# Optimization experiments

Measured on AMD Instinct MI355X. Metric: run time of the kernel, lower is better.

Reference implementation:

```python
import jax, jax.numpy as jnp
import numpy as np

SAMPLE_THRESH = 0.05  # self.sample_thresh


def grid_sample_bilinear_zeros(img, pts):
    """torch.nn.functional.grid_sample with mode='bilinear', align_corners=False,
    padding_mode='zeros'. img: [C, H, W]; pts: [N, 2] with (x, y) in [-1, 1].
    Returns [C, N]."""
    C, H, W = img.shape
    # align_corners=False unnormalization
    x = (pts[:, 0] + 1.0) * (W / 2.0) - 0.5
    y = (pts[:, 1] + 1.0) * (H / 2.0) - 0.5
    x0 = jnp.floor(x)
    y0 = jnp.floor(y)
    wx1 = x - x0
    wy1 = y - y0
    wx0 = 1.0 - wx1
    wy0 = 1.0 - wy1

    def gather(xi, yi):
        valid = (xi >= 0) & (xi < W) & (yi >= 0) & (yi < H)
        xi_c = jnp.clip(xi, 0, W - 1).astype(jnp.int32)
        yi_c = jnp.clip(yi, 0, H - 1).astype(jnp.int32)
        v = img[:, yi_c, xi_c]  # [C, N]
        return v * valid.astype(img.dtype)[None, :]

    out = (gather(x0, y0) * (wx0 * wy0)[None, :]
           + gather(x0 + 1, y0) * (wx1 * wy0)[None, :]
           + gather(x0, y0 + 1) * (wx0 * wy1)[None, :]
           + gather(x0 + 1, y0 + 1) * (wx1 * wy1)[None, :])
    return out


def setup_inputs() -> dict:
    key = jax.random.key(0)
    k1, k2, k3, k4 = jax.random.split(key, 4)
    N_A, N_B = 8192, 8192
    H, W2 = 504, 1008  # warp is [hs, 2*ws, 4] per post_process
    x_A = jax.random.uniform(k1, (N_A, 2), jnp.float32, -1.0, 1.0)
    x_B = jax.random.uniform(k2, (N_B, 2), jnp.float32, -1.0, 1.0)
    warp = jax.random.uniform(k3, (H, W2, 4), jnp.float32, -1.0, 1.0)
    certainty = jax.random.uniform(k4, (H, W2), jnp.float32, 0.0, 1.0)
    return {"x_A": x_A, "x_B": x_B, "warp": warp, "certainty": certainty}


def reference(x_A, x_B, warp, certainty):
    # --- match_keypoints ---
    # x_A_to_B = grid_sample(warp[..., -2:].permute(2,0,1)[None], x_A[None,None])[0,:,0].mT
    flow_img = jnp.transpose(warp[..., -2:], (2, 0, 1))  # [2, H, 2W]
    x_A_to_B = grid_sample_bilinear_zeros(flow_img, x_A).T  # [N_A, 2]
    cert_A_to_B = grid_sample_bilinear_zeros(certainty[None], x_A)[0]  # [N_A]

    # D = torch.cdist(x_A_to_B, x_B) via |a|^2 + |b|^2 - 2 a.b
    a2 = jnp.sum(x_A_to_B * x_A_to_B, axis=-1)  # [N_A]
    b2 = jnp.sum(x_B * x_B, axis=-1)            # [N_B]
    D2 = a2[:, None] + b2[None, :] - 2.0 * (x_A_to_B @ x_B.T)
    D = jnp.sqrt(jnp.maximum(D2, 1e-12))  # [N_A, N_B]

    # mutual nearest-neighbor mask with certainty threshold
    row_min = jnp.min(D, axis=-1, keepdims=True)
    col_min = jnp.min(D, axis=-2, keepdims=True)
    mask = (D == row_min) & (D == col_min) & (cert_A_to_B[:, None] > SAMPLE_THRESH)

    # jit-compatible equivalent of torch.nonzero: distances at mutual-NN pairs,
    # zero elsewhere. nonzero entries == matched (inds_A, inds_B) pairs.
    return jnp.where(mask, D, 0.0)
```

## Files before the change

### kernel.cpp

```cpp
#include <hip/hip_runtime.h>
#include <math.h>

#define SAMPLE_THRESH 0.05f

__device__ __forceinline__ float d2_exact(float xa0, float xa1, float a2,
                                          float xb0, float xb1, float b2) {
    float p  = __fmul_rn(xa1, xb1);
    float q  = __fmaf_rn(xa0, xb0, p);
    float s  = __fadd_rn(a2, b2);
    return __fmaf_rn(-2.0f, q, s);
}

__device__ __forceinline__ float D_from_d2(float d2) {
    return __fsqrt_rn(fmaxf(d2, 1e-12f));
}

__global__ __launch_bounds__(256) void sample_kernel(
    const float* __restrict__ xA, const float* __restrict__ xB,
    const float4* __restrict__ warp, const float* __restrict__ cert,
    float4* __restrict__ Apack, float4* __restrict__ Bpack,
    int nA, int nB, int H, int W) {
    int i = blockIdx.x * blockDim.x + threadIdx.x;
    if (i < nA) {
        float px = xA[2 * i + 0], py = xA[2 * i + 1];
        float xf = (px + 1.0f) * (0.5f * (float)W) - 0.5f;
        float yf = (py + 1.0f) * (0.5f * (float)H) - 0.5f;
        float x0f = floorf(xf), y0f = floorf(yf);
        float wx1 = xf - x0f, wy1 = yf - y0f;
        float wx0 = 1.0f - wx1, wy0 = 1.0f - wy1;
        int x0 = (int)x0f, y0 = (int)y0f;
        float fx = 0.0f, fy = 0.0f, cv = 0.0f;
#pragma unroll
        for (int dy = 0; dy < 2; ++dy) {
#pragma unroll
            for (int dx = 0; dx < 2; ++dx) {
                int xi = x0 + dx, yi = y0 + dy;
                float vm = (xi >= 0 && xi < W && yi >= 0 && yi < H) ? 1.0f : 0.0f;
                int xc = min(max(xi, 0), W - 1);
                int yc = min(max(yi, 0), H - 1);
                int idx = yc * W + xc;
                float4 wv = warp[idx];
                float  c  = cert[idx];
                float wgt = (dx ? wx1 : wx0) * (dy ? wy1 : wy0);
                fx += (wv.z * vm) * wgt;
                fy += (wv.w * vm) * wgt;
                cv += (c    * vm) * wgt;
            }
        }
        float a2 = fx * fx + fy * fy;
        Apack[i] = make_float4(fx, fy, a2, cv);
    }
    if (i < nB) {
        float b0 = xB[2 * i + 0], b1 = xB[2 * i + 1];
        Bpack[i] = make_float4(b0, b1, b0 * b0 + b1 * b1, 0.0f);
    }
}

#define MROWS 8
__global__ __launch_bounds__(256) void min_kernel(
    const float4* __restrict__ Apack, const float4* __restrict__ Bpack,
    float4* __restrict__ rowpack, float4* __restrict__ colpack,
    int nA, int nB) {
    int gwave = (int)((blockIdx.x * blockDim.x + threadIdx.x) >> 6);
    int lane = threadIdx.x & 63;
    int nRowWaves = nA / MROWS;
    float m[MROWS];
#pragma unroll
    for (int r = 0; r < MROWS; ++r) m[r] = 1e30f;
    if (gwave < nRowWaves) {
        int i0 = gwave * MROWS;
        float4 A[MROWS];
#pragma unroll
        for (int r = 0; r < MROWS; ++r) A[r] = Apack[i0 + r];
        for (int j = lane; j < nB; j += 64) {
            float4 b = Bpack[j];
#pragma unroll
            for (int r = 0; r < MROWS; ++r)
                m[r] = fminf(m[r], d2_exact(A[r].x, A[r].y, A[r].z, b.x, b.y, b.z));
        }
#pragma unroll
        for (int o = 32; o; o >>= 1) {
#pragma unroll
            for (int r = 0; r < MROWS; ++r)
                m[r] = fminf(m[r], __shfl_xor(m[r], o, 64));
        }
        if (lane == 0) {
#pragma unroll
            for (int r = 0; r < MROWS; ++r)
                rowpack[i0 + r] = make_float4(A[r].x, A[r].y, A[r].z,
                    (A[r].w > SAMPLE_THRESH) ? D_from_d2(m[r]) : -1.0f);
        }
    } else {
        int j0 = (gwave - nRowWaves) * MROWS;
        if (j0 >= nB) return;
        float4 B[MROWS];
#pragma unroll
        for (int r = 0; r < MROWS; ++r) B[r] = Bpack[j0 + r];
        for (int i = lane; i < nA; i += 64) {
            float4 a = Apack[i];
#pragma unroll
            for (int r = 0; r < MROWS; ++r)
                m[r] = fminf(m[r], d2_exact(a.x, a.y, a.z, B[r].x, B[r].y, B[r].z));
        }
#pragma unroll
        for (int o = 32; o; o >>= 1) {
#pragma unroll
            for (int r = 0; r < MROWS; ++r)
                m[r] = fminf(m[r], __shfl_xor(m[r], o, 64));
        }
        if (lane == 0) {
#pragma unroll
            for (int r = 0; r < MROWS; ++r)
                colpack[j0 + r] = make_float4(B[r].x, B[r].y, B[r].z, D_from_d2(m[r]));
        }
    }
}

#define TI 64
#define TJ 1024
__global__ __launch_bounds__(256) void out_kernel(
    const float4* __restrict__ rowpack, const float4* __restrict__ colpack,
    float* __restrict__ out, int N) {
    __shared__ float4 cp[TJ];
    __shared__ float4 rp[TI];
    int tid = threadIdx.x;
    int j0 = blockIdx.x * TJ;
    int i0 = blockIdx.y * TI;
    for (int k = tid; k < TJ; k += 256) cp[k] = colpack[j0 + k];
    if (tid < TI) rp[tid] = rowpack[i0 + tid];
    __syncthreads();
    float4 c0 = cp[tid * 4 + 0], c1 = cp[tid * 4 + 1];
    float4 c2 = cp[tid * 4 + 2], c3 = cp[tid * 4 + 3];
    size_t base = (size_t)i0 * (size_t)N + (size_t)j0 + (size_t)tid * 4;
    for (int r = 0; r < TI; ++r) {
        float4 a = rp[r];
        float d0 = D_from_d2(d2_exact(a.x, a.y, a.z, c0.x, c0.y, c0.z));
        float d1 = D_from_d2(d2_exact(a.x, a.y, a.z, c1.x, c1.y, c1.z));
        float d2 = D_from_d2(d2_exact(a.x, a.y, a.z, c2.x, c2.y, c2.z));
        float d3 = D_from_d2(d2_exact(a.x, a.y, a.z, c3.x, c3.y, c3.z));
        float4 o;
        o.x = (d0 == a.w && d0 == c0.w) ? d0 : 0.0f;
        o.y = (d1 == a.w && d1 == c1.w) ? d1 : 0.0f;
        o.z = (d2 == a.w && d2 == c2.w) ? d2 : 0.0f;
        o.w = (d3 == a.w && d3 == c3.w) ? d3 : 0.0f;
        *(float4*)(out + base + (size_t)r * (size_t)N) = o;
    }
}

extern "C" void kernel_launch(void* const* d_in, const int* in_sizes, int n_in,
                              void* d_out, int out_size, void* d_ws, size_t ws_size,
                              hipStream_t stream) {
    const float* xA   = (const float*)d_in[0];
    const float* xB   = (const float*)d_in[1];
    const float* warp = (const float*)d_in[2];
    const float* cert = (const float*)d_in[3];
    int nA = in_sizes[0] / 2;
    int nB = in_sizes[1] / 2;
    const int H = 504, W = 1008;
    float* out = (float*)d_out;

    char* ws = (char*)d_ws;
    float4* Apack   = (float4*)ws;
    float4* Bpack   = Apack + nA;
    float4* rowpack = Bpack + nB;
    float4* colpack = rowpack + nA;

    int nmax = nA > nB ? nA : nB;
    sample_kernel<<<(nmax + 255) / 256, 256, 0, stream>>>(
        xA, xB, (const float4*)warp, cert, Apack, Bpack, nA, nB, H, W);

    int totWaves = nA / MROWS + nB / MROWS;
    min_kernel<<<(totWaves * 64 + 255) / 256, 256, 0, stream>>>(
        Apack, Bpack, rowpack, colpack, nA, nB);

    dim3 grid(nB / TJ, nA / TI);
    out_kernel<<<grid, 256, 0, stream>>>(rowpack, colpack, out, nB);
}
```

Baseline: 333.1 us.

## Compute row and column minima in one tiled pass with atomicMin

Replaces the separate row-wise and column-wise minimum scans with a single 128x128 tiled pair kernel. Each distance is computed once and feeds both row and column minima. Results are merged across blocks via atomicMin on order-preserving unsigned float encodings, initialized in the sample kernel. The output kernel now rebuilds the row and column metadata from the packed points and the atomic minima. This halves the distance arithmetic at the cost of global atomics and extra shuffles.

```diff
diff --git a/kernel.cpp b/kernel.cpp
--- a/kernel.cpp
+++ b/kernel.cpp
@@ -15,13 +15,23 @@
     return __fsqrt_rn(fmaxf(d2, 1e-12f));
 }
 
+__device__ __forceinline__ unsigned flipf(float f) {
+    unsigned u = __float_as_uint(f);
+    return (u & 0x80000000u) ? ~u : (u | 0x80000000u);
+}
+__device__ __forceinline__ float unflipf(unsigned u) {
+    return __uint_as_float((u & 0x80000000u) ? (u ^ 0x80000000u) : ~u);
+}
+
 __global__ __launch_bounds__(256) void sample_kernel(
     const float* __restrict__ xA, const float* __restrict__ xB,
     const float4* __restrict__ warp, const float* __restrict__ cert,
     float4* __restrict__ Apack, float4* __restrict__ Bpack,
+    unsigned* __restrict__ rowmin_u, unsigned* __restrict__ colmin_u,
     int nA, int nB, int H, int W) {
     int i = blockIdx.x * blockDim.x + threadIdx.x;
     if (i < nA) {
+        rowmin_u[i] = 0xFFFFFFFFu;
         float px = xA[2 * i + 0], py = xA[2 * i + 1];
         float xf = (px + 1.0f) * (0.5f * (float)W) - 0.5f;
         float yf = (py + 1.0f) * (0.5f * (float)H) - 0.5f;
@@ -51,83 +61,98 @@
         Apack[i] = make_float4(fx, fy, a2, cv);
     }
     if (i < nB) {
+        colmin_u[i] = 0xFFFFFFFFu;
         float b0 = xB[2 * i + 0], b1 = xB[2 * i + 1];
         Bpack[i] = make_float4(b0, b1, b0 * b0 + b1 * b1, 0.0f);
     }
 }
 
-#define MROWS 8
-__global__ __launch_bounds__(256) void min_kernel(
+#define BM 128
+#define BN 128
+__global__ __launch_bounds__(256) void pair_kernel(
     const float4* __restrict__ Apack, const float4* __restrict__ Bpack,
-    float4* __restrict__ rowpack, float4* __restrict__ colpack,
-    int nA, int nB) {
-    int gwave = (int)((blockIdx.x * blockDim.x + threadIdx.x) >> 6);
-    int lane = threadIdx.x & 63;
-    int nRowWaves = nA / MROWS;
-    float m[MROWS];
-#pragma unroll
-    for (int r = 0; r < MROWS; ++r) m[r] = 1e30f;
-    if (gwave < nRowWaves) {
-        int i0 = gwave * MROWS;
-        float4 A[MROWS];
-#pragma unroll
-        for (int r = 0; r < MROWS; ++r) A[r] = Apack[i0 + r];
-        for (int j = lane; j < nB; j += 64) {
-            float4 b = Bpack[j];
-#pragma unroll
-            for (int r = 0; r < MROWS; ++r)
-                m[r] = fminf(m[r], d2_exact(A[r].x, A[r].y, A[r].z, b.x, b.y, b.z));
+    unsigned* __restrict__ rowmin_u, unsigned* __restrict__ colmin_u) {
+    __shared__ float4 At[BM];
+    __shared__ float4 Bt[BN + BN / 8];
+    __shared__ unsigned colred[BN];
+    int t = threadIdx.x;
+    int i0 = blockIdx.y * BM, j0 = blockIdx.x * BN;
+    if (t < BM) {
+        At[t] = Apack[i0 + t];
+        colred[t] = 0xFFFFFFFFu;
+    } else {
+        int j = t - BM;
+        Bt[j + (j >> 3)] = Bpack[j0 + j];
+    }
+    __syncthreads();
+    int tx = t & 15, ty = t >> 4;
+    float ax[8], ay[8], az[8], bx[8], by[8], bz[8];
+#pragma unroll
+    for (int r = 0; r < 8; ++r) {
+        float4 a = At[ty * 8 + r];
+        ax[r] = a.x; ay[r] = a.y; az[r] = a.z;
+    }
+#pragma unroll
+    for (int c = 0; c < 8; ++c) {
+        float4 b = Bt[tx * 9 + c];
+        bx[c] = b.x; by[c] = b.y; bz[c] = b.z;
+    }
+    float rmin[8], cmin[8];
+#pragma unroll
+    for (int r = 0; r < 8; ++r) { rmin[r] = 1e30f; cmin[r] = 1e30f; }
+#pragma unroll
+    for (int r = 0; r < 8; ++r) {
+#pragma unroll
+        for (int c = 0; c < 8; ++c) {
+            float d2 = d2_exact(ax[r], ay[r], az[r], bx[c], by[c], bz[c]);
+            rmin[r] = fminf(rmin[r], d2);
+            cmin[c] = fminf(cmin[c], d2);
         }
-#pragma unroll
-        for (int o = 32; o; o >>= 1) {
-#pragma unroll
-            for (int r = 0; r < MROWS; ++r)
-                m[r] = fminf(m[r], __shfl_xor(m[r], o, 64));
-        }
-        if (lane == 0) {
-#pragma unroll
-            for (int r = 0; r < MROWS; ++r)
-                rowpack[i0 + r] = make_float4(A[r].x, A[r].y, A[r].z,
-                    (A[r].w > SAMPLE_THRESH) ? D_from_d2(m[r]) : -1.0f);
-        }
-    } else {
-        int j0 = (gwave - nRowWaves) * MROWS;
-        if (j0 >= nB) return;
-        float4 B[MROWS];
-#pragma unroll
-        for (int r = 0; r < MROWS; ++r) B[r] = Bpack[j0 + r];
-        for (int i = lane; i < nA; i += 64) {
-            float4 a = Apack[i];
-#pragma unroll
-            for (int r = 0; r < MROWS; ++r)
-                m[r] = fminf(m[r], d2_exact(a.x, a.y, a.z, B[r].x, B[r].y, B[r].z));
-        }
-#pragma unroll
-        for (int o = 32; o; o >>= 1) {
-#pragma unroll
-            for (int r = 0; r < MROWS; ++r)
-                m[r] = fminf(m[r], __shfl_xor(m[r], o, 64));
-        }
-        if (lane == 0) {
-#pragma unroll
-            for (int r = 0; r < MROWS; ++r)
-                colpack[j0 + r] = make_float4(B[r].x, B[r].y, B[r].z, D_from_d2(m[r]));
-        }
-    }
+    }
+#pragma unroll
+    for (int o = 1; o <= 8; o <<= 1)
+#pragma unroll
+        for (int r = 0; r < 8; ++r)
+            rmin[r] = fminf(rmin[r], __shfl_xor(rmin[r], o, 64));
+    if (tx == 0) {
+#pragma unroll
+        for (int r = 0; r < 8; ++r)
+            atomicMin(&rowmin_u[i0 + ty * 8 + r], flipf(rmin[r]));
+    }
+#pragma unroll
+    for (int o = 16; o <= 32; o <<= 1)
+#pragma unroll
+        for (int c = 0; c < 8; ++c)
+            cmin[c] = fminf(cmin[c], __shfl_xor(cmin[c], o, 64));
+    if ((t & 63) < 16) {
+#pragma unroll
+        for (int c = 0; c < 8; ++c)
+            atomicMin(&colred[tx * 8 + c], flipf(cmin[c]));
+    }
+    __syncthreads();
+    if (t < BN) atomicMin(&colmin_u[j0 + t], colred[t]);
 }
 
 #define TI 64
 #define TJ 1024
 __global__ __launch_bounds__(256) void out_kernel(
-    const float4* __restrict__ rowpack, const float4* __restrict__ colpack,
+    const float4* __restrict__ Apack, const float4* __restrict__ Bpack,
+    const unsigned* __restrict__ rowmin_u, const unsigned* __restrict__ colmin_u,
     float* __restrict__ out, int N) {
     __shared__ float4 cp[TJ];
     __shared__ float4 rp[TI];
     int tid = threadIdx.x;
     int j0 = blockIdx.x * TJ;
     int i0 = blockIdx.y * TI;
-    for (int k = tid; k < TJ; k += 256) cp[k] = colpack[j0 + k];
-    if (tid < TI) rp[tid] = rowpack[i0 + tid];
+    for (int k = tid; k < TJ; k += 256) {
+        float4 b = Bpack[j0 + k];
+        cp[k] = make_float4(b.x, b.y, b.z, D_from_d2(unflipf(colmin_u[j0 + k])));
+    }
+    if (tid < TI) {
+        float4 a = Apack[i0 + tid];
+        rp[tid] = make_float4(a.x, a.y, a.z,
+            (a.w > SAMPLE_THRESH) ? D_from_d2(unflipf(rowmin_u[i0 + tid])) : -1.0f);
+    }
     __syncthreads();
     float4 c0 = cp[tid * 4 + 0], c1 = cp[tid * 4 + 1];
     float4 c2 = cp[tid * 4 + 2], c3 = cp[tid * 4 + 3];
@@ -160,19 +185,19 @@
     float* out = (float*)d_out;
 
     char* ws = (char*)d_ws;
-    float4* Apack   = (float4*)ws;
-    float4* Bpack   = Apack + nA;
-    float4* rowpack = Bpack + nB;
-    float4* colpack = rowpack + nA;
+    float4*   Apack    = (float4*)ws;
+    float4*   Bpack    = Apack + nA;
+    unsigned* rowmin_u = (unsigned*)(Bpack + nB);
+    unsigned* colmin_u = rowmin_u + nA;
 
     int nmax = nA > nB ? nA : nB;
     sample_kernel<<<(nmax + 255) / 256, 256, 0, stream>>>(
-        xA, xB, (const float4*)warp, cert, Apack, Bpack, nA, nB, H, W);
-
-    int totWaves = nA / MROWS + nB / MROWS;
-    min_kernel<<<(totWaves * 64 + 255) / 256, 256, 0, stream>>>(
-        Apack, Bpack, rowpack, colpack, nA, nB);
-
-    dim3 grid(nB / TJ, nA / TI);
-    out_kernel<<<grid, 256, 0, stream>>>(rowpack, colpack, out, nB);
-}
+        xA, xB, (const float4*)warp, cert, Apack, Bpack,
+        rowmin_u, colmin_u, nA, nB, H, W);
+
+    dim3 pgrid(nB / BN, nA / BM);
+    pair_kernel<<<pgrid, 256, 0, stream>>>(Apack, Bpack, rowmin_u, colmin_u);
+
+    dim3 ogrid(nB / TJ, nA / TI);
+    out_kernel<<<ogrid, 256, 0, stream>>>(Apack, Bpack, rowmin_u, colmin_u, out, nB);
+}
```

Measured after the change: 321.4 us. 1.04x faster.
